# Optimization experiments

Measured on AMD Instinct MI355X. Metric: run time of the kernel, lower is better.

The kernel has to match this reference:

```python
import jax, jax.numpy as jnp
import numpy as np

N = 50000   # nodes
E = 800000  # edges (avg degree 16)
IN = 64     # in_dim
DS = 32     # in_dim // 2
HOUT = 64


def setup_inputs() -> dict:
    key = jax.random.key(0)
    ks = jax.random.split(key, 16)
    std = 0.1

    def w(k, shape):
        return std * jax.random.normal(k, shape, dtype=jnp.float32)

    z = lambda d: jnp.zeros((d,), dtype=jnp.float32)
    return {
        "x": jax.random.normal(ks[0], (N, IN), dtype=jnp.float32),
        "src": jax.random.randint(ks[1], (E,), 0, N),
        "dst": jax.random.randint(ks[2], (E,), 0, N),
        # encoders (enc_dim == in_dim branch: dim_split -> dim_split)
        "WencK": w(ks[3], (DS, DS)), "bencK": z(DS),
        "WencP1": w(ks[4], (DS, DS)), "bencP1": z(DS),
        "WencP2": w(ks[5], (DS, DS)), "bencP2": z(DS),
        # Kfun MLP: Linear(DS,HOUT) Tanh Linear(HOUT,HOUT) ReLU Linear(HOUT,HOUT)
        "WK1": w(ks[6], (DS, HOUT)), "bK1": z(HOUT),
        "WK2": w(ks[7], (HOUT, HOUT)), "bK2": z(HOUT),
        "WK3": w(ks[8], (HOUT, HOUT)), "bK3": z(HOUT),
        # Ufun MLP (same structure)
        "WU1": w(ks[9], (DS, HOUT)), "bU1": z(HOUT),
        "WU2": w(ks[10], (HOUT, HOUT)), "bU2": z(HOUT),
        "WU3": w(ks[11], (HOUT, HOUT)), "bU3": z(HOUT),
        # output heads
        "WH": w(ks[12], (HOUT, IN)), "bH": z(IN),
        "WD": w(ks[13], (IN, IN)), "bD": z(IN),
    }


def _mlp3(h, W1, b1, W2, b2, W3, b3):
    h = jnp.tanh(h @ W1 + b1)
    h = jax.nn.relu(h @ W2 + b2)
    return h @ W3 + b3


def reference(x, src, dst,
              WencK, bencK, WencP1, bencP1, WencP2, bencP2,
              WK1, bK1, WK2, bK2, WK3, bK3,
              WU1, bU1, WU2, bU2, WU3, bU3,
              WH, bH, WD, bD):
    ds = DS
    q, p = x[:, :ds], x[:, ds:]

    # getK: encode p, scatter-sum over incoming edges, node MLP
    hK = p @ WencK + bencK                              # [N, DS]
    hK_agg = jax.ops.segment_sum(hK[src], dst, num_segments=N)
    E_node = _mlp3(hK_agg, WK1, bK1, WK2, bK2, WK3, bK3)  # [N, HOUT]

    # getU: u_add_v on encoded q, edge MLP
    h1 = q @ WencP1 + bencP1
    h2 = q @ WencP2 + bencP2
    e_out = h1[src] + h2[dst]                           # [E, DS]
    E_edge = _mlp3(e_out, WU1, bU1, WU2, bU2, WU3, bU3)  # [E, HOUT]

    # getH: u_mul_e then sum into destination nodes
    E_new = jax.ops.segment_sum(E_node[src] * E_edge, dst, num_segments=N)

    # dHdx
    dH = E_new @ WH + bH                                # [N, IN]

    # get_D: dissipation term on second half of D(x), scattered over graph
    Dx = x @ WD + bD
    d_agg = jax.ops.segment_sum(Dx[:, ds:][src], dst, num_segments=N)
    d = jnp.concatenate([jnp.zeros_like(d_agg), d_agg], axis=-1)

    # dH @ J^T with J = [[0, I], [-I, 0]]  ->  [dH_p, -dH_q]
    out = jnp.concatenate([dH[:, ds:], -dH[:, :ds]], axis=-1) - d
    return out
```

## Files before the change

### kernel.cpp

```cpp
#include <hip/hip_runtime.h>
#include <hip/hip_bf16.h>

#define NN 50000
#define EE 800000
#define IN_DIM 64
#define DS_DIM 32
#define HOUT_DIM 64

#define K4_WAVES 10000
#define K4_EPW   80
#define K4_C     5
#define K4_NWG   (K4_WAVES / 4)

#define XA_EPW 64
#define XA_NWG 3125

#define HIST_BLOCKS 3125
#define ENC_BLOCKS  6250

#define SCAN_NB 196

#define XPS 72

typedef __attribute__((ext_vector_type(8))) short bf16x8;
typedef __attribute__((ext_vector_type(4))) float f32x4;

__device__ __forceinline__ float fast_tanh(float x) {
    float e = __builtin_amdgcn_exp2f(x * 2.885390082f);
    return 1.f - 2.f * __builtin_amdgcn_rcpf(e + 1.f);
}

__device__ __forceinline__ void atomAddF(float* p, float v) {
#if defined(__AMDGCN__)
    unsafeAtomicAdd(p, v);
#else
    atomicAdd(p, v);
#endif
}

__device__ __forceinline__ short f2b(float f) {
    union { __hip_bfloat16 h; short s; } u;
    u.h = __float2bfloat16(f);
    return u.s;
}
__device__ __forceinline__ float b2f(unsigned short u) {
    return __uint_as_float(((unsigned int)u) << 16);
}
__device__ __forceinline__ unsigned int pack2(float lo, float hi) {
    return (unsigned int)(unsigned short)f2b(lo) | (((unsigned int)(unsigned short)f2b(hi)) << 16);
}

__device__ __forceinline__ int xcd_swz(int bid, int nwg) {
    int xcd = bid & 7, idx = bid >> 3;
    int q = nwg >> 3, r = nwg & 7;
    return (xcd < r ? xcd * (q + 1) : r * (q + 1) + (xcd - r) * q) + idx;
}

__global__ void kmega0(const int* __restrict__ dst, int* __restrict__ cnt, int* __restrict__ rank,
                       const float* __restrict__ x,
                       const float* __restrict__ WencP1, const float* __restrict__ bencP1,
                       const float* __restrict__ WencP2, const float* __restrict__ bencP2,
                       __hip_bfloat16* __restrict__ h1b, __hip_bfloat16* __restrict__ h2b,
                       __hip_bfloat16* __restrict__ xb) {
    if (blockIdx.x < HIST_BLOCKS) {
        int e = blockIdx.x * 256 + threadIdx.x;
        rank[e] = atomicAdd(&cnt[dst[e]], 1);
    } else {
        int tid = (blockIdx.x - HIST_BLOCKS) * 256 + threadIdx.x;
        int n = tid >> 5;
        int j = tid & 31;
        if (n >= NN) return;
        const float* xr = x + (size_t)n * IN_DIM;
        float a1 = bencP1[j], a2 = bencP2[j];
        #pragma unroll
        for (int k = 0; k < 32; k++) {
            float q = xr[k];
            a1 = fmaf(q, WencP1[k * 32 + j], a1);
            a2 = fmaf(q, WencP2[k * 32 + j], a2);
        }
        union { __hip_bfloat16 h; short s; } u1, u2, u3, u4;
        u1.s = f2b(a1); u2.s = f2b(a2);
        h1b[(size_t)n * 32 + j] = u1.h;
        h2b[(size_t)n * 32 + j] = u2.h;
        u3.s = f2b(xr[j]); u4.s = f2b(xr[32 + j]);
        xb[(size_t)n * 64 + j] = u3.h;
        xb[(size_t)n * 64 + 32 + j] = u4.h;
    }
}

__global__ void kscanA(const int* __restrict__ cnt, int* __restrict__ blocksum) {
    __shared__ int s[256];
    int t = threadIdx.x;
    int i = blockIdx.x * 256 + t;
    s[t] = (i < NN) ? cnt[i] : 0;
    __syncthreads();
    #pragma unroll
    for (int off = 128; off > 0; off >>= 1) {
        if (t < off) s[t] += s[t + off];
        __syncthreads();
    }
    if (t == 0) blocksum[blockIdx.x] = s[0];
}

__global__ void kscanB(const int* __restrict__ blocksum, int* __restrict__ blockoff) {
    __shared__ int part[256];
    int t = threadIdx.x;
    int v = (t < SCAN_NB) ? blocksum[t] : 0;
    part[t] = v;
    __syncthreads();
    for (int off = 1; off < 256; off <<= 1) {
        int u = (t >= off) ? part[t - off] : 0;
        __syncthreads();
        part[t] += u;
        __syncthreads();
    }
    if (t < SCAN_NB) blockoff[t] = part[t] - v;
}

__global__ void kscanC(const int* __restrict__ cnt, const int* __restrict__ blockoff,
                       int* __restrict__ rowptr, int* __restrict__ dstp) {
    __shared__ int part[256];
    int t = threadIdx.x;
    int i = blockIdx.x * 256 + t;
    int v = (i < NN) ? cnt[i] : 0;
    part[t] = v;
    __syncthreads();
    for (int off = 1; off < 256; off <<= 1) {
        int u = (t >= off) ? part[t - off] : 0;
        __syncthreads();
        part[t] += u;
        __syncthreads();
    }
    if (i < NN) {
        int incl = blockoff[blockIdx.x] + part[t];
        int lo = incl - v;
        rowptr[i] = lo;
        if (i == NN - 1) rowptr[NN] = incl;
        for (int p = lo; p < incl; p++) dstp[p] = i;
    }
}

__global__ void kscatter(const int* __restrict__ src, const int* __restrict__ dst,
                         const int* __restrict__ rowptr, const int* __restrict__ rank,
                         int* __restrict__ srcp) {
    int e = blockIdx.x * 256 + threadIdx.x;
    if (e >= EE) return;
    int d = dst[e];
    srcp[rowptr[d] + rank[e]] = src[e];
}

__global__ void __launch_bounds__(256) kxagg3(const int* __restrict__ srcp,
                                              const int* __restrict__ dstp,
                                              const __hip_bfloat16* __restrict__ xb,
                                              float* __restrict__ xagg) {
    int sbid = xcd_swz(blockIdx.x, XA_NWG);
    int w = sbid * 4 + (threadIdx.x >> 6);
    int lane = threadIdx.x & 63;
    int base = w * XA_EPW;
    const unsigned short* xu = reinterpret_cast<const unsigned short*>(xb);

    int sarr = srcp[base + lane];
    int darr = dstp[base + lane];

    float v0 = b2f(xu[(size_t)__shfl(sarr, 0) * 64 + lane]);
    float v1 = b2f(xu[(size_t)__shfl(sarr, 1) * 64 + lane]);
    float v2 = b2f(xu[(size_t)__shfl(sarr, 2) * 64 + lane]);
    float v3 = b2f(xu[(size_t)__shfl(sarr, 3) * 64 + lane]);
    int cd = __shfl(darr, 0);
    float carry = 0.f;

#define XA_STEP(vv, T)                                                        \
    {                                                                         \
        float cur = vv;                                                       \
        if ((T) + 4 < XA_EPW)                                                 \
            vv = b2f(xu[(size_t)__shfl(sarr, (T) + 4) * 64 + lane]);          \
        int d = __shfl(darr, (T));                                            \
        if (d != cd) {                                                        \
            atomAddF(&xagg[(size_t)cd * 64 + lane], carry);                   \
            cd = d; carry = 0.f;                                              \
        }                                                                     \
        carry += cur;                                                         \
    }

    for (int tb = 0; tb < XA_EPW; tb += 4) {
        XA_STEP(v0, tb);
        XA_STEP(v1, tb + 1);
        XA_STEP(v2, tb + 2);
        XA_STEP(v3, tb + 3);
    }
#undef XA_STEP
    atomAddF(&xagg[(size_t)cd * 64 + lane], carry);
}

__global__ void __launch_bounds__(256) k3ab(
    const float* __restrict__ xagg, const int* __restrict__ cnt,
    const float* __restrict__ WencK, const float* __restrict__ bencK,
    const float* __restrict__ WD, const float* __restrict__ bD,
    const float* __restrict__ WK1, const float* __restrict__ bK1,
    const float* __restrict__ WK2, const float* __restrict__ bK2,
    const float* __restrict__ WK3, const float* __restrict__ bK3,
    float* __restrict__ dagg, __hip_bfloat16* __restrict__ EnodeT)
{
    __shared__ unsigned short xpose[4][16 * XPS];
    const int wid  = threadIdx.x >> 6;
    const int lane = threadIdx.x & 63;
    const int g = lane >> 4;
    const int r = lane & 15;
    unsigned short* xp = xpose[wid];

    bf16x8 bwd[2][2];
    #pragma unroll
    for (int c = 0; c < 2; c++)
        #pragma unroll
        for (int nd = 0; nd < 2; nd++)
            #pragma unroll
            for (int i = 0; i < 8; i++)
                bwd[c][nd][i] = f2b(WD[(c * 32 + g * 8 + i) * 64 + 32 + nd * 16 + r]);
    bf16x8 bwk[2];
    #pragma unroll
    for (int nd = 0; nd < 2; nd++)
        #pragma unroll
        for (int i = 0; i < 8; i++)
            bwk[nd][i] = f2b(WencK[(g * 8 + i) * 32 + nd * 16 + r]);
    bf16x8 b1[4];
    #pragma unroll
    for (int nt = 0; nt < 4; nt++)
        #pragma unroll
        for (int i = 0; i < 8; i++)
            b1[nt][i] = f2b(WK1[(g * 8 + i) * 64 + nt * 16 + r]);
    bf16x8 b2[2][4], b3[2][4];
    #pragma unroll
    for (int c = 0; c < 2; c++)
        #pragma unroll
        for (int nt = 0; nt < 4; nt++)
            #pragma unroll
            for (int i = 0; i < 8; i++) {
                b2[c][nt][i] = f2b(WK2[(c * 32 + g * 8 + i) * 64 + nt * 16 + r]);
                b3[c][nt][i] = f2b(WK3[(c * 32 + g * 8 + i) * 64 + nt * 16 + r]);
            }
    float bdv[2], bkv[2];
    #pragma unroll
    for (int nd = 0; nd < 2; nd++) {
        bdv[nd] = bD[32 + nd * 16 + r];
        bkv[nd] = bencK[nd * 16 + r];
    }
    float bias1[4], bias2[4], bias3[4];
    #pragma unroll
    for (int nt = 0; nt < 4; nt++) {
        bias1[nt] = bK1[nt * 16 + r];
        bias2[nt] = bK2[nt * 16 + r];
        bias3[nt] = bK3[nt * 16 + r];
    }

    const int ntiles = NN / 16;
    const int wave = blockIdx.x * 4 + wid;
    const int nw = gridDim.x * 4;
    const f32x4 zero = {0.f, 0.f, 0.f, 0.f};

    for (int tile = wave; tile < ntiles; tile += nw) {
        bf16x8 ax0, ax1;
        {
            const float* xr = xagg + ((size_t)tile * 16 + r) * 64 + g * 8;
            float4 p0 = *reinterpret_cast<const float4*>(xr);
            float4 p1 = *reinterpret_cast<const float4*>(xr + 4);
            float4 p2 = *reinterpret_cast<const float4*>(xr + 32);
            float4 p3 = *reinterpret_cast<const float4*>(xr + 36);
            ax0[0] = f2b(p0.x); ax0[1] = f2b(p0.y); ax0[2] = f2b(p0.z); ax0[3] = f2b(p0.w);
            ax0[4] = f2b(p1.x); ax0[5] = f2b(p1.y); ax0[6] = f2b(p1.z); ax0[7] = f2b(p1.w);
            ax1[0] = f2b(p2.x); ax1[1] = f2b(p2.y); ax1[2] = f2b(p2.z); ax1[3] = f2b(p2.w);
            ax1[4] = f2b(p3.x); ax1[5] = f2b(p3.y); ax1[6] = f2b(p3.z); ax1[7] = f2b(p3.w);
        }
        float cq[4];
        #pragma unroll
        for (int q = 0; q < 4; q++) cq[q] = (float)cnt[tile * 16 + g * 4 + q];

        f32x4 accd[2];
        #pragma unroll
        for (int nd = 0; nd < 2; nd++) {
            accd[nd] = __builtin_amdgcn_mfma_f32_16x16x32_bf16(ax0, bwd[0][nd], zero, 0, 0, 0);
            accd[nd] = __builtin_amdgcn_mfma_f32_16x16x32_bf16(ax1, bwd[1][nd], accd[nd], 0, 0, 0);
        }
        #pragma unroll
        for (int nd = 0; nd < 2; nd++)
            #pragma unroll
            for (int q = 0; q < 4; q++)
                dagg[((size_t)tile * 16 + g * 4 + q) * 32 + nd * 16 + r] =
                    accd[nd][q] + cq[q] * bdv[nd];

        f32x4 acch[2];
        #pragma unroll
        for (int nd = 0; nd < 2; nd++)
            acch[nd] = __builtin_amdgcn_mfma_f32_16x16x32_bf16(ax1, bwk[nd], zero, 0, 0, 0);
        #pragma unroll
        for (int nd = 0; nd < 2; nd++)
            #pragma unroll
            for (int q = 0; q < 4; q++)
                xp[(g * 4 + q) * XPS + nd * 16 + r] = (unsigned short)f2b(acch[nd][q] + cq[q] * bkv[nd]);

        bf16x8 af = *reinterpret_cast<const bf16x8*>(xp + r * XPS + g * 8);
        f32x4 acc[4];
        #pragma unroll
        for (int nt = 0; nt < 4; nt++)
            acc[nt] = __builtin_amdgcn_mfma_f32_16x16x32_bf16(af, b1[nt], zero, 0, 0, 0);
        #pragma unroll
        for (int nt = 0; nt < 4; nt++)
            #pragma unroll
            for (int q = 0; q < 4; q++)
                xp[(g * 4 + q) * XPS + nt * 16 + r] = (unsigned short)f2b(fast_tanh(acc[nt][q] + bias1[nt]));

        f32x4 acc2[4] = {zero, zero, zero, zero};
        #pragma unroll
        for (int c = 0; c < 2; c++) {
            bf16x8 a2 = *reinterpret_cast<const bf16x8*>(xp + r * XPS + c * 32 + g * 8);
            #pragma unroll
            for (int nt = 0; nt < 4; nt++)
                acc2[nt] = __builtin_amdgcn_mfma_f32_16x16x32_bf16(a2, b2[c][nt], acc2[nt], 0, 0, 0);
        }
        #pragma unroll
        for (int nt = 0; nt < 4; nt++)
            #pragma unroll
            for (int q = 0; q < 4; q++)
                xp[(g * 4 + q) * XPS + nt * 16 + r] = (unsigned short)f2b(fmaxf(acc2[nt][q] + bias2[nt], 0.f));

        f32x4 acc3[4] = {zero, zero, zero, zero};
        #pragma unroll
        for (int c = 0; c < 2; c++) {
            bf16x8 a3 = *reinterpret_cast<const bf16x8*>(xp + r * XPS + c * 32 + g * 8);
            #pragma unroll
            for (int nt = 0; nt < 4; nt++)
                acc3[nt] = __builtin_amdgcn_mfma_f32_16x16x32_bf16(a3, b3[c][nt], acc3[nt], 0, 0, 0);
        }
        #pragma unroll
        for (int q = 0; q < 4; q++) {
            uint2 v;
            v.x = pack2(acc3[0][q] + bias3[0], acc3[1][q] + bias3[1]);
            v.y = pack2(acc3[2][q] + bias3[2], acc3[3][q] + bias3[3]);
            *reinterpret_cast<uint2*>(reinterpret_cast<unsigned short*>(EnodeT)
                + ((size_t)tile * 16 + g * 4 + q) * 64 + r * 4) = v;
        }
    }
}

__global__ void __launch_bounds__(256) k4_mfma(
    const int* __restrict__ srcp, const int* __restrict__ dstp,
    const __hip_bfloat16* __restrict__ h1b, const __hip_bfloat16* __restrict__ h2b,
    const __hip_bfloat16* __restrict__ EnodeT, float* __restrict__ Enew,
    const float* __restrict__ WU1, const float* __restrict__ bU1,
    const float* __restrict__ WU2, const float* __restrict__ bU2,
    const float* __restrict__ WU3, const float* __restrict__ bU3)
{
    __shared__ unsigned short xpose[4][16 * XPS];
    const int wid  = threadIdx.x >> 6;
    const int lane = threadIdx.x & 63;
    const int g = lane >> 4;
    const int r = lane & 15;
    unsigned short* xp = xpose[wid];

    bf16x8 b1[4];
    #pragma unroll
    for (int nt = 0; nt < 4; nt++) {
        #pragma unroll
        for (int i = 0; i < 8; i++)
            b1[nt][i] = f2b(WU1[(g * 8 + i) * 64 + nt * 16 + r]);
    }
    bf16x8 b2[2][4], b3[2][4];
    #pragma unroll
    for (int c = 0; c < 2; c++) {
        #pragma unroll
        for (int nt = 0; nt < 4; nt++) {
            #pragma unroll
            for (int i = 0; i < 8; i++) {
                b2[c][nt][i] = f2b(WU2[(c * 32 + g * 8 + i) * 64 + nt * 16 + r]);
                b3[c][nt][i] = f2b(WU3[(c * 32 + g * 8 + i) * 64 + nt * 16 + r]);
            }
        }
    }
    float bias1[4], bias2[4], bias3[4];
    #pragma unroll
    for (int nt = 0; nt < 4; nt++) {
        bias1[nt] = bU1[nt * 16 + r];
        bias2[nt] = bU2[nt * 16 + r];
        bias3[nt] = bU3[nt * 16 + r];
    }

    const int sbid = xcd_swz(blockIdx.x, K4_NWG);
    const int wave = sbid * 4 + wid;
    const int base = wave * K4_EPW;
    const f32x4 zero = {0.f, 0.f, 0.f, 0.f};
    const unsigned short* enT = reinterpret_cast<const unsigned short*>(EnodeT);

    int   cd[4] = {-1, -1, -1, -1};
    float cv0[4] = {0, 0, 0, 0}, cv1[4] = {0, 0, 0, 0},
          cv2[4] = {0, 0, 0, 0}, cv3[4] = {0, 0, 0, 0};

    int sp = srcp[base + r * K4_C];
    int dp = dstp[base + r * K4_C];
    uint4 v1 = *reinterpret_cast<const uint4*>(h1b + (size_t)sp * 32 + g * 8);
    uint4 v2 = *reinterpret_cast<const uint4*>(h2b + (size_t)dp * 32 + g * 8);

    for (int t = 0; t < K4_C; t++) {
        const int s_me = sp, d_me = dp;
        union { uint4 v; bf16x8 b; } ua1, ua2;
        ua1.v = v1; ua2.v = v2;
        if (t + 1 < K4_C) {
            sp = srcp[base + r * K4_C + t + 1];
            dp = dstp[base + r * K4_C + t + 1];
            v1 = *reinterpret_cast<const uint4*>(h1b + (size_t)sp * 32 + g * 8);
            v2 = *reinterpret_cast<const uint4*>(h2b + (size_t)dp * 32 + g * 8);
        }

        int dq[4];
        float en0[4], en1[4], en2[4], en3[4];
        #pragma unroll
        for (int q = 0; q < 4; q++) {
            const int er = g * 4 + q;
            const int ssv = __shfl(s_me, er);
            dq[q] = __shfl(d_me, er);
            uint2 ev = *reinterpret_cast<const uint2*>(enT + (size_t)ssv * 64 + r * 4);
            en0[q] = b2f((unsigned short)(ev.x & 0xffff));
            en1[q] = b2f((unsigned short)(ev.x >> 16));
            en2[q] = b2f((unsigned short)(ev.y & 0xffff));
            en3[q] = b2f((unsigned short)(ev.y >> 16));
        }

        __builtin_amdgcn_s_setprio(1);
        f32x4 acc[4];
        #pragma unroll
        for (int nt = 0; nt < 4; nt++) {
            acc[nt] = __builtin_amdgcn_mfma_f32_16x16x32_bf16(ua2.b, b1[nt], zero, 0, 0, 0);
            acc[nt] = __builtin_amdgcn_mfma_f32_16x16x32_bf16(ua1.b, b1[nt], acc[nt], 0, 0, 0);
        }

        #pragma unroll
        for (int nt = 0; nt < 4; nt++) {
            #pragma unroll
            for (int q = 0; q < 4; q++)
                xp[(g * 4 + q) * XPS + nt * 16 + r] = (unsigned short)f2b(fast_tanh(acc[nt][q] + bias1[nt]));
        }

        f32x4 acc2[4] = {zero, zero, zero, zero};
        #pragma unroll
        for (int c = 0; c < 2; c++) {
            bf16x8 af = *reinterpret_cast<const bf16x8*>(xp + r * XPS + c * 32 + g * 8);
            #pragma unroll
            for (int nt = 0; nt < 4; nt++)
                acc2[nt] = __builtin_amdgcn_mfma_f32_16x16x32_bf16(af, b2[c][nt], acc2[nt], 0, 0, 0);
        }
        #pragma unroll
        for (int nt = 0; nt < 4; nt++) {
            #pragma unroll
            for (int q = 0; q < 4; q++)
                xp[(g * 4 + q) * XPS + nt * 16 + r] = (unsigned short)f2b(fmaxf(acc2[nt][q] + bias2[nt], 0.f));
        }

        f32x4 acc3[4] = {zero, zero, zero, zero};
        #pragma unroll
        for (int c = 0; c < 2; c++) {
            bf16x8 af = *reinterpret_cast<const bf16x8*>(xp + r * XPS + c * 32 + g * 8);
            #pragma unroll
            for (int nt = 0; nt < 4; nt++)
                acc3[nt] = __builtin_amdgcn_mfma_f32_16x16x32_bf16(af, b3[c][nt], acc3[nt], 0, 0, 0);
        }
        __builtin_amdgcn_s_setprio(0);

        #pragma unroll
        for (int q = 0; q < 4; q++) {
            float w0 = (acc3[0][q] + bias3[0]) * en0[q];
            float w1 = (acc3[1][q] + bias3[1]) * en1[q];
            float w2 = (acc3[2][q] + bias3[2]) * en2[q];
            float w3 = (acc3[3][q] + bias3[3]) * en3[q];
            if (dq[q] == cd[q]) {
                cv0[q] += w0; cv1[q] += w1; cv2[q] += w2; cv3[q] += w3;
            } else {
                if (cd[q] >= 0) {
                    float* ew = Enew + (size_t)cd[q] * 64 + r;
                    atomAddF(ew,      cv0[q]);
                    atomAddF(ew + 16, cv1[q]);
                    atomAddF(ew + 32, cv2[q]);
                    atomAddF(ew + 48, cv3[q]);
                }
                cd[q] = dq[q];
                cv0[q] = w0; cv1[q] = w1; cv2[q] = w2; cv3[q] = w3;
            }
        }
    }
    #pragma unroll
    for (int q = 0; q < 4; q++) {
        if (cd[q] >= 0) {
            float* ew = Enew + (size_t)cd[q] * 64 + r;
            atomAddF(ew,      cv0[q]);
            atomAddF(ew + 16, cv1[q]);
            atomAddF(ew + 32, cv2[q]);
            atomAddF(ew + 48, cv3[q]);
        }
    }
}

__global__ void k5_out(const float* __restrict__ Enew, const float* __restrict__ dagg,
                       const float* __restrict__ WH, const float* __restrict__ bH,
                       float* __restrict__ out) {
    int tid = blockIdx.x * blockDim.x + threadIdx.x;
    int n = tid >> 6;
    int j = tid & 63;
    if (n >= NN) return;
    const float* er = Enew + (size_t)n * 64;
    int jj = (j < 32) ? (j + 32) : (j - 32);
    float acc = bH[jj];
    #pragma unroll
    for (int k = 0; k < 64; k++) acc = fmaf(er[k], WH[k * 64 + jj], acc);
    float val;
    if (j < 32) val = acc;
    else        val = -acc - dagg[(size_t)n * 32 + (j - 32)];
    out[tid] = val;
}

extern "C" void kernel_launch(void* const* d_in, const int* in_sizes, int n_in,
                              void* d_out, int out_size, void* d_ws, size_t ws_size,
                              hipStream_t stream) {
    const float* x      = (const float*)d_in[0];
    const int*   src    = (const int*)d_in[1];
    const int*   dst    = (const int*)d_in[2];
    const float* WencK  = (const float*)d_in[3];
    const float* bencK  = (const float*)d_in[4];
    const float* WencP1 = (const float*)d_in[5];
    const float* bencP1 = (const float*)d_in[6];
    const float* WencP2 = (const float*)d_in[7];
    const float* bencP2 = (const float*)d_in[8];
    const float* WK1    = (const float*)d_in[9];
    const float* bK1    = (const float*)d_in[10];
    const float* WK2    = (const float*)d_in[11];
    const float* bK2    = (const float*)d_in[12];
    const float* WK3    = (const float*)d_in[13];
    const float* bK3    = (const float*)d_in[14];
    const float* WU1    = (const float*)d_in[15];
    const float* bU1    = (const float*)d_in[16];
    const float* WU2    = (const float*)d_in[17];
    const float* bU2    = (const float*)d_in[18];
    const float* WU3    = (const float*)d_in[19];
    const float* bU3    = (const float*)d_in[20];
    const float* WH     = (const float*)d_in[21];
    const float* bH     = (const float*)d_in[22];
    const float* WD     = (const float*)d_in[23];
    const float* bD     = (const float*)d_in[24];
    float* out = (float*)d_out;

    float* xagg = (float*)d_ws;
    float* Enew = xagg + (size_t)NN * 64;
    float* dagg = Enew + (size_t)NN * 64;
    __hip_bfloat16* h1b    = (__hip_bfloat16*)(dagg + (size_t)NN * 32);
    __hip_bfloat16* h2b    = h1b + (size_t)NN * 32;
    __hip_bfloat16* EnodeT = h2b + (size_t)NN * 32;
    __hip_bfloat16* xb     = EnodeT + (size_t)NN * 64;
    int*  cnt      = (int*)(xb + (size_t)NN * 64);
    int*  rowptr   = cnt + NN;
    int*  blocksum = rowptr + NN + 2;
    int*  blockoff = blocksum + 256;
    int*  rank     = blockoff + 256;
    int*  srcp     = rank + EE;
    int*  dstp     = srcp + EE;
    size_t need = (size_t)NN * 160 * 4 + (size_t)NN * 192 * 2
                + ((size_t)NN * 2 + 2 + 512) * 4 + (size_t)EE * 12;
    if (ws_size < need) return;

    hipMemsetAsync(cnt, 0, (size_t)NN * sizeof(int), stream);
    hipMemsetAsync(xagg, 0, (size_t)NN * 128 * sizeof(float), stream);

    kmega0<<<HIST_BLOCKS + ENC_BLOCKS, 256, 0, stream>>>(
        dst, cnt, rank, x, WencP1, bencP1, WencP2, bencP2, h1b, h2b, xb);
    kscanA<<<SCAN_NB, 256, 0, stream>>>(cnt, blocksum);
    kscanB<<<1, 256, 0, stream>>>(blocksum, blockoff);
    kscanC<<<SCAN_NB, 256, 0, stream>>>(cnt, blockoff, rowptr, dstp);
    kscatter<<<HIST_BLOCKS, 256, 0, stream>>>(src, dst, rowptr, rank, srcp);
    kxagg3<<<XA_NWG, 256, 0, stream>>>(srcp, dstp, xb, xagg);
    k3ab<<<782, 256, 0, stream>>>(xagg, cnt, WencK, bencK, WD, bD,
                                  WK1, bK1, WK2, bK2, WK3, bK3, dagg, EnodeT);
    k4_mfma<<<K4_NWG, 256, 0, stream>>>(srcp, dstp, h1b, h2b, EnodeT, Enew,
                                        WU1, bU1, WU2, bU2, WU3, bU3);
    k5_out<<<(NN * 64 + 255) / 256, 256, 0, stream>>>(Enew, dagg, WH, bH, out);
}
```

Measured before the change: 253.9 us.

## Fuse CSR neighbor aggregation into node MLP kernel via shared-memory accumulators

Removes the separate atomic-based neighbor aggregation kernel and its global fp32 xagg buffer. Each wave now walks the CSR-sorted edges of its 16-node tile, accumulates sums in LDS without atomics, and feeds them straight into the MFMA node pipeline. Degree comes from rowptr differences instead of the cnt array. This saves a kernel launch, the atomics, the memset of xagg and a global round trip. In exchange the gather phase is serial within each wave and tiles with uneven edge counts can cause load imbalance across 782 blocks.

```diff
diff --git a/kernel.cpp b/kernel.cpp
--- a/kernel.cpp
+++ b/kernel.cpp
@@ -12,15 +12,13 @@
 #define K4_C     5
 #define K4_NWG   (K4_WAVES / 4)
 
-#define XA_EPW 64
-#define XA_NWG 3125
-
 #define HIST_BLOCKS 3125
 #define ENC_BLOCKS  6250
 
 #define SCAN_NB 196
 
 #define XPS 72
+#define ACS 68
 
 typedef __attribute__((ext_vector_type(8))) short bf16x8;
 typedef __attribute__((ext_vector_type(4))) float f32x4;
@@ -149,51 +147,10 @@
     srcp[rowptr[d] + rank[e]] = src[e];
 }
 
-__global__ void __launch_bounds__(256) kxagg3(const int* __restrict__ srcp,
-                                              const int* __restrict__ dstp,
-                                              const __hip_bfloat16* __restrict__ xb,
-                                              float* __restrict__ xagg) {
-    int sbid = xcd_swz(blockIdx.x, XA_NWG);
-    int w = sbid * 4 + (threadIdx.x >> 6);
-    int lane = threadIdx.x & 63;
-    int base = w * XA_EPW;
-    const unsigned short* xu = reinterpret_cast<const unsigned short*>(xb);
-
-    int sarr = srcp[base + lane];
-    int darr = dstp[base + lane];
-
-    float v0 = b2f(xu[(size_t)__shfl(sarr, 0) * 64 + lane]);
-    float v1 = b2f(xu[(size_t)__shfl(sarr, 1) * 64 + lane]);
-    float v2 = b2f(xu[(size_t)__shfl(sarr, 2) * 64 + lane]);
-    float v3 = b2f(xu[(size_t)__shfl(sarr, 3) * 64 + lane]);
-    int cd = __shfl(darr, 0);
-    float carry = 0.f;
-
-#define XA_STEP(vv, T)                                                        \
-    {                                                                         \
-        float cur = vv;                                                       \
-        if ((T) + 4 < XA_EPW)                                                 \
-            vv = b2f(xu[(size_t)__shfl(sarr, (T) + 4) * 64 + lane]);          \
-        int d = __shfl(darr, (T));                                            \
-        if (d != cd) {                                                        \
-            atomAddF(&xagg[(size_t)cd * 64 + lane], carry);                   \
-            cd = d; carry = 0.f;                                              \
-        }                                                                     \
-        carry += cur;                                                         \
-    }
-
-    for (int tb = 0; tb < XA_EPW; tb += 4) {
-        XA_STEP(v0, tb);
-        XA_STEP(v1, tb + 1);
-        XA_STEP(v2, tb + 2);
-        XA_STEP(v3, tb + 3);
-    }
-#undef XA_STEP
-    atomAddF(&xagg[(size_t)cd * 64 + lane], carry);
-}
-
-__global__ void __launch_bounds__(256) k3ab(
-    const float* __restrict__ xagg, const int* __restrict__ cnt,
+__global__ void __launch_bounds__(256) kmega2(
+    const int* __restrict__ rowptr,
+    const int* __restrict__ srcp, const int* __restrict__ dstp,
+    const __hip_bfloat16* __restrict__ xb,
     const float* __restrict__ WencK, const float* __restrict__ bencK,
     const float* __restrict__ WD, const float* __restrict__ bD,
     const float* __restrict__ WK1, const float* __restrict__ bK1,
@@ -201,12 +158,15 @@
     const float* __restrict__ WK3, const float* __restrict__ bK3,
     float* __restrict__ dagg, __hip_bfloat16* __restrict__ EnodeT)
 {
+    __shared__ float accs[4][16 * ACS];
     __shared__ unsigned short xpose[4][16 * XPS];
     const int wid  = threadIdx.x >> 6;
     const int lane = threadIdx.x & 63;
     const int g = lane >> 4;
     const int r = lane & 15;
+    float* accL = accs[wid];
     unsigned short* xp = xpose[wid];
+    const unsigned short* xu = reinterpret_cast<const unsigned short*>(xb);
 
     bf16x8 bwd[2][2];
     #pragma unroll
@@ -258,21 +218,51 @@
     const f32x4 zero = {0.f, 0.f, 0.f, 0.f};
 
     for (int tile = wave; tile < ntiles; tile += nw) {
+        const int bn = tile * 16;
+        #pragma unroll
+        for (int i = 0; i < 16; i++) accL[i * ACS + lane] = 0.f;
+
+        const int lo = rowptr[bn], hi = rowptr[bn + 16];
+        int cd = -1;
+        float carry = 0.f;
+        for (int cb = lo; cb < hi; cb += 64) {
+            int myp = cb + lane;
+            bool valid = myp < hi;
+            int sarr = valid ? srcp[myp] : 0;
+            int darr = valid ? dstp[myp] : 0;
+            int cnum = hi - cb; if (cnum > 64) cnum = 64;
+            int s0 = __shfl(sarr, 0);
+            float v = b2f(xu[(size_t)s0 * 64 + lane]);
+            for (int t = 0; t < cnum; t++) {
+                float cur = v;
+                if (t + 1 < cnum) {
+                    int sn = __shfl(sarr, t + 1);
+                    v = b2f(xu[(size_t)sn * 64 + lane]);
+                }
+                int d = __shfl(darr, t);
+                if (d != cd) {
+                    if (cd >= 0) accL[(cd - bn) * ACS + lane] = carry;
+                    cd = d; carry = 0.f;
+                }
+                carry += cur;
+            }
+        }
+        if (cd >= 0) accL[(cd - bn) * ACS + lane] = carry;
+
         bf16x8 ax0, ax1;
         {
-            const float* xr = xagg + ((size_t)tile * 16 + r) * 64 + g * 8;
-            float4 p0 = *reinterpret_cast<const float4*>(xr);
-            float4 p1 = *reinterpret_cast<const float4*>(xr + 4);
-            float4 p2 = *reinterpret_cast<const float4*>(xr + 32);
-            float4 p3 = *reinterpret_cast<const float4*>(xr + 36);
-            ax0[0] = f2b(p0.x); ax0[1] = f2b(p0.y); ax0[2] = f2b(p0.z); ax0[3] = f2b(p0.w);
-            ax0[4] = f2b(p1.x); ax0[5] = f2b(p1.y); ax0[6] = f2b(p1.z); ax0[7] = f2b(p1.w);
-            ax1[0] = f2b(p2.x); ax1[1] = f2b(p2.y); ax1[2] = f2b(p2.z); ax1[3] = f2b(p2.w);
-            ax1[4] = f2b(p3.x); ax1[5] = f2b(p3.y); ax1[6] = f2b(p3.z); ax1[7] = f2b(p3.w);
+            const float* ar = accL + r * ACS + g * 8;
+            #pragma unroll
+            for (int i = 0; i < 8; i++) ax0[i] = f2b(ar[i]);
+            #pragma unroll
+            for (int i = 0; i < 8; i++) ax1[i] = f2b(ar[32 + i]);
         }
         float cq[4];
         #pragma unroll
-        for (int q = 0; q < 4; q++) cq[q] = (float)cnt[tile * 16 + g * 4 + q];
+        for (int q = 0; q < 4; q++) {
+            int n = bn + g * 4 + q;
+            cq[q] = (float)(rowptr[n + 1] - rowptr[n]);
+        }
 
         f32x4 accd[2];
         #pragma unroll
@@ -284,7 +274,7 @@
         for (int nd = 0; nd < 2; nd++)
             #pragma unroll
             for (int q = 0; q < 4; q++)
-                dagg[((size_t)tile * 16 + g * 4 + q) * 32 + nd * 16 + r] =
+                dagg[((size_t)bn + g * 4 + q) * 32 + nd * 16 + r] =
                     accd[nd][q] + cq[q] * bdv[nd];
 
         f32x4 acch[2];
@@ -336,7 +326,7 @@
             v.x = pack2(acc3[0][q] + bias3[0], acc3[1][q] + bias3[1]);
             v.y = pack2(acc3[2][q] + bias3[2], acc3[3][q] + bias3[3]);
             *reinterpret_cast<uint2*>(reinterpret_cast<unsigned short*>(EnodeT)
-                + ((size_t)tile * 16 + g * 4 + q) * 64 + r * 4) = v;
+                + ((size_t)bn + g * 4 + q) * 64 + r * 4) = v;
         }
     }
 }
@@ -544,8 +534,7 @@
     const float* bD     = (const float*)d_in[24];
     float* out = (float*)d_out;
 
-    float* xagg = (float*)d_ws;
-    float* Enew = xagg + (size_t)NN * 64;
+    float* Enew = (float*)d_ws;
     float* dagg = Enew + (size_t)NN * 64;
     __hip_bfloat16* h1b    = (__hip_bfloat16*)(dagg + (size_t)NN * 32);
     __hip_bfloat16* h2b    = h1b + (size_t)NN * 32;
@@ -558,12 +547,12 @@
     int*  rank     = blockoff + 256;
     int*  srcp     = rank + EE;
     int*  dstp     = srcp + EE;
-    size_t need = (size_t)NN * 160 * 4 + (size_t)NN * 192 * 2
+    size_t need = (size_t)NN * 96 * 4 + (size_t)NN * 192 * 2
                 + ((size_t)NN * 2 + 2 + 512) * 4 + (size_t)EE * 12;
     if (ws_size < need) return;
 
     hipMemsetAsync(cnt, 0, (size_t)NN * sizeof(int), stream);
-    hipMemsetAsync(xagg, 0, (size_t)NN * 128 * sizeof(float), stream);
+    hipMemsetAsync(Enew, 0, (size_t)NN * 64 * sizeof(float), stream);
 
     kmega0<<<HIST_BLOCKS + ENC_BLOCKS, 256, 0, stream>>>(
         dst, cnt, rank, x, WencP1, bencP1, WencP2, bencP2, h1b, h2b, xb);
@@ -571,9 +560,8 @@
     kscanB<<<1, 256, 0, stream>>>(blocksum, blockoff);
     kscanC<<<SCAN_NB, 256, 0, stream>>>(cnt, blockoff, rowptr, dstp);
     kscatter<<<HIST_BLOCKS, 256, 0, stream>>>(src, dst, rowptr, rank, srcp);
-    kxagg3<<<XA_NWG, 256, 0, stream>>>(srcp, dstp, xb, xagg);
-    k3ab<<<782, 256, 0, stream>>>(xagg, cnt, WencK, bencK, WD, bD,
-                                  WK1, bK1, WK2, bK2, WK3, bK3, dagg, EnodeT);
+    kmega2<<<782, 256, 0, stream>>>(rowptr, srcp, dstp, xb, WencK, bencK, WD, bD,
+                                    WK1, bK1, WK2, bK2, WK3, bK3, dagg, EnodeT);
     k4_mfma<<<K4_NWG, 256, 0, stream>>>(srcp, dstp, h1b, h2b, EnodeT, Enew,
                                         WU1, bU1, WU2, bU2, WU3, bU3);
     k5_out<<<(NN * 64 + 255) / 256, 256, 0, stream>>>(Enew, dagg, WH, bH, out);
```

After: 425.7 us. +67.7%, slower.
